# Kernel optimization log

Measured on AMD Instinct MI355X. Metric: run time of the kernel, lower is better.

The kernel has to match this reference:

```python
import jax, jax.numpy as jnp
import numpy as np

N, H, O, E, K = 131072, 128, 128, 8, 2


def setup_inputs() -> dict:
    key = jax.random.key(0)
    k1, k2, k3, k4 = jax.random.split(key, 4)
    x = jax.random.normal(k1, (N, H), dtype=jnp.float32)
    w_gate = jax.random.normal(k2, (H, E), dtype=jnp.float32) * 0.02
    w_noise = jax.random.normal(k3, (H, E), dtype=jnp.float32) * 0.02
    w_expert = jax.random.normal(k4, (E, H, O), dtype=jnp.float32) * (1.0 / np.sqrt(H))
    b_expert = jnp.zeros((E, O), dtype=jnp.float32)
    return {"x": x, "w_gate": w_gate, "w_noise": w_noise,
            "w_expert": w_expert, "b_expert": b_expert, "top_k": K}


def _gates(x, w_gate, top_k):
    # Noisy top-k gating (eval mode: noise term w_noise is inactive).
    logits = x @ w_gate                              # [N, E]
    top_vals, top_idx = jax.lax.top_k(logits, top_k)  # [N, K]
    top_gates = jax.nn.softmax(top_vals, axis=-1)     # renormalize over top-k
    n = logits.shape[0]
    rows = jnp.arange(n)[:, None]                     # [N, 1]
    gates = jnp.zeros_like(logits).at[rows, top_idx].set(top_gates)  # [N, E] sparse
    return gates


def reference(x, w_gate, w_noise, w_expert, b_expert, top_k):
    gates = _gates(x, w_gate, top_k)                                  # [N, E]
    # Dense (mathematically identical) dispatch/combine: every expert FFN
    # applied per token, weighted by its (mostly-zero) gate.
    expert_out = jnp.einsum('nh,eho->neo', x, w_expert) + b_expert     # [N, E, O]
    out = jnp.einsum('ne,neo->no', gates, expert_out)                  # [N, O]
    return out
```

## Files before the change

kernel.cpp:

```cpp
#include <hip/hip_runtime.h>
#include <math.h>

typedef __bf16 bf16x8 __attribute__((ext_vector_type(8)));
typedef float f32x16 __attribute__((ext_vector_type(16)));

#define NTOK 131072
#define HDIM 128
#define ODIM 128
#define NEXP 8

__device__ __forceinline__ unsigned short f2bf(float f){
  union { float f; unsigned u; } v; v.f = f;
  unsigned r = v.u + 0x7FFFu + ((v.u >> 16) & 1u);
  return (unsigned short)(r >> 16);
}

__global__ void pack_w(const float* __restrict__ we, const float* __restrict__ be,
                       unsigned short* __restrict__ pw){
  int f = blockIdx.x * 256 + threadIdx.x;
  int l  = f & 63;
  int kt = (f >> 6) % 9;
  int emt = f / (64 * 9);
  int mt = emt & 3;
  int e  = emt >> 2;
  int o  = (mt << 5) + (l & 31);
  unsigned short vals[8];
#pragma unroll
  for (int j = 0; j < 8; ++j){
    int kl = ((l >> 5) << 3) + j;
    float v;
    if (kt < 8){
      int h = kt * 16 + kl;
      v = we[(e * HDIM + h) * ODIM + o];
    } else {
      v = (kl == 0) ? be[e * ODIM + o] : 0.0f;
    }
    vals[j] = f2bf(v);
  }
  *(bf16x8*)(pw + (size_t)f * 8) = *(bf16x8*)vals;
}

__launch_bounds__(256, 2)
__global__ void moe_fused(const float* __restrict__ x, const float* __restrict__ wg,
                          const unsigned short* __restrict__ pw, float* __restrict__ out){
  __shared__ char lds[33792 + 4096 + 2048];
  float* xs            = (float*)lds;
  unsigned short* frag = (unsigned short*)lds;
  float* tb            = (float*)lds;
  float* wgl           = (float*)(lds + 33792);
  float* glds          = (float*)(lds + 33792 + 4096);

  int t = threadIdx.x;
  size_t tokbase = (size_t)blockIdx.x * 64;

  ((float4*)wgl)[t] = ((const float4*)wg)[t];
  {
    const float4* xsrc = (const float4*)(x + tokbase * HDIM);
#pragma unroll
    for (int i = 0; i < 8; ++i){
      int idx = i * 256 + t;
      int tok = idx >> 5, c = idx & 31;
      *(float4*)&xs[tok * 132 + c * 4] = xsrc[idx];
    }
  }
  __syncthreads();

  float4 cv[8];
#pragma unroll
  for (int i = 0; i < 8; ++i)
    cv[i] = *(float4*)&xs[(t >> 2) * 132 + (t & 3) * 32 + i * 4];

  if (t < 64){
    float lg[8];
#pragma unroll
    for (int e = 0; e < 8; ++e) lg[e] = 0.0f;
#pragma unroll 8
    for (int c = 0; c < 32; ++c){
      float4 v = *(float4*)&xs[t * 132 + c * 4];
      const float* wr = wgl + c * 32;
#pragma unroll
      for (int e = 0; e < 8; ++e)
        lg[e] += v.x * wr[e] + v.y * wr[8 + e] + v.z * wr[16 + e] + v.w * wr[24 + e];
    }
    int i1 = 0; float v1 = lg[0];
#pragma unroll
    for (int e = 1; e < 8; ++e) if (lg[e] > v1){ v1 = lg[e]; i1 = e; }
    int i2 = -1; float v2 = -3.4e38f;
#pragma unroll
    for (int e = 0; e < 8; ++e) if (e != i1 && lg[e] > v2){ v2 = lg[e]; i2 = e; }
    float ex = __expf(v2 - v1);
    float inv = 1.0f / (1.0f + ex);
#pragma unroll
    for (int e = 0; e < 8; ++e)
      glds[e * 64 + t] = (e == i1) ? inv : ((e == i2) ? ex * inv : 0.0f);
  }
  __syncthreads();

  {
    int tokL = t >> 2, q = t & 3, tg = tokL >> 5;
#pragma unroll
    for (int jb = 0; jb < 4; ++jb){
      int h0 = q * 32 + jb * 8;
      int kt = h0 >> 4;
      int lslot = (tokL & 31) + 32 * ((h0 >> 3) & 1);
      float4 a = cv[2 * jb], b = cv[2 * jb + 1];
      unsigned long long lo = (unsigned long long)f2bf(a.x)
                            | ((unsigned long long)f2bf(a.y) << 16)
                            | ((unsigned long long)f2bf(a.z) << 32)
                            | ((unsigned long long)f2bf(a.w) << 48);
      unsigned long long hi = (unsigned long long)f2bf(b.x)
                            | ((unsigned long long)f2bf(b.y) << 16)
                            | ((unsigned long long)f2bf(b.z) << 32)
                            | ((unsigned long long)f2bf(b.w) << 48);
      unsigned long long* dst =
        (unsigned long long*)&frag[(((tg * 9) + kt) * 64 + lslot) * 8];
      dst[0] = lo; dst[1] = hi;
    }
    if (t < 128){
      int btg = t >> 6, bl = t & 63;
      unsigned long long* dst =
        (unsigned long long*)&frag[(((btg * 9) + 8) * 64 + bl) * 8];
      dst[0] = (bl < 32) ? 0x3F80ull : 0ull;
      dst[1] = 0ull;
    }
  }
  __syncthreads();

  int w = t >> 6, l = t & 63, l32 = l & 31, lh = l >> 5;

  bf16x8 xb0[9], xb1[9];
#pragma unroll
  for (int kt = 0; kt < 9; ++kt){
    xb0[kt] = *(const bf16x8*)&frag[((0 * 9 + kt) * 64 + l) * 8];
    xb1[kt] = *(const bf16x8*)&frag[((1 * 9 + kt) * 64 + l) * 8];
  }
  __syncthreads();

  f32x16 zero16;
#pragma unroll
  for (int i = 0; i < 16; ++i) zero16[i] = 0.0f;
  f32x16 tot0 = zero16, tot1 = zero16;

  const bf16x8* pwp = (const bf16x8*)pw;
#pragma unroll 1
  for (int e = 0; e < 8; ++e){
    float g0 = glds[e * 64 + l32];
    float g1 = glds[e * 64 + 32 + l32];
    const bf16x8* ap = pwp + ((size_t)(e * 4 + w) * 9) * 64 + l;
    f32x16 p0 = zero16, p1 = zero16;
#pragma unroll
    for (int kt = 0; kt < 9; ++kt){
      bf16x8 a = ap[kt * 64];
      p0 = __builtin_amdgcn_mfma_f32_32x32x16_bf16(a, xb0[kt], p0, 0, 0, 0);
      p1 = __builtin_amdgcn_mfma_f32_32x32x16_bf16(a, xb1[kt], p1, 0, 0, 0);
    }
#pragma unroll
    for (int r = 0; r < 16; ++r){
      tot0[r] += g0 * p0[r];
      tot1[r] += g1 * p1[r];
    }
  }

  {
#pragma unroll
    for (int rg = 0; rg < 4; ++rg){
      int o = w * 32 + rg * 8 + lh * 4;
      {
        int trow = 0 * 32 + l32;
        int cs = (o >> 2) ^ l32;
        *(float4*)&tb[trow * 128 + cs * 4] =
          make_float4(tot0[rg * 4 + 0], tot0[rg * 4 + 1], tot0[rg * 4 + 2], tot0[rg * 4 + 3]);
      }
      {
        int trow = 1 * 32 + l32;
        int cs = (o >> 2) ^ l32;
        *(float4*)&tb[trow * 128 + cs * 4] =
          make_float4(tot1[rg * 4 + 0], tot1[rg * 4 + 1], tot1[rg * 4 + 2], tot1[rg * 4 + 3]);
      }
    }
  }
  __syncthreads();
#pragma unroll
  for (int i = 0; i < 8; ++i){
    int idx = i * 256 + t;
    int trow = idx >> 5, c = idx & 31;
    int cs = c ^ (trow & 31);
    float4 v = *(float4*)&tb[trow * 128 + cs * 4];
    *(float4*)(out + (tokbase + trow) * ODIM + c * 4) = v;
  }
}

extern "C" void kernel_launch(void* const* d_in, const int* in_sizes, int n_in,
                              void* d_out, int out_size, void* d_ws, size_t ws_size,
                              hipStream_t stream){
  const float* x  = (const float*)d_in[0];
  const float* wg = (const float*)d_in[1];
  const float* we = (const float*)d_in[3];
  const float* be = (const float*)d_in[4];
  float* out = (float*)d_out;

  unsigned short* pw = (unsigned short*)d_ws;

  pack_w   <<<72,   256, 0, stream>>>(we, be, pw);
  moe_fused<<<2048, 256, 0, stream>>>(x, wg, pw, out);
}
```

Baseline: 161.3 us.

## Spread gate logit computation across all threads and prefetch gates into registers

Gate logits were computed by only 64 threads, each doing all 8 experts. Now all 256 threads each compute 2 experts for one token, using a transposed copy of w_gate in LDS, and write the logits to LDS before a single thread-group does top-k and softmax. Gate values are loaded into registers before the expert loop, and the loop is unrolled by 2 so weight loads can overlap across experts. This adds a barrier and the LDS transposed stores, and the unroll raises register pressure under the 2-waves launch bound.

```diff
diff --git a/kernel.cpp b/kernel.cpp
--- a/kernel.cpp
+++ b/kernel.cpp
@@ -47,13 +47,20 @@
   float* xs            = (float*)lds;
   unsigned short* frag = (unsigned short*)lds;
   float* tb            = (float*)lds;
-  float* wgl           = (float*)(lds + 33792);
+  float* wgt           = (float*)(lds + 33792);
   float* glds          = (float*)(lds + 33792 + 4096);
 
   int t = threadIdx.x;
   size_t tokbase = (size_t)blockIdx.x * 64;
 
-  ((float4*)wgl)[t] = ((const float4*)wg)[t];
+  {
+    float4 v = ((const float4*)wg)[t];
+    int h = t >> 1, e0 = (t & 1) * 4;
+    wgt[(e0 + 0) * 128 + h] = v.x;
+    wgt[(e0 + 1) * 128 + h] = v.y;
+    wgt[(e0 + 2) * 128 + h] = v.z;
+    wgt[(e0 + 3) * 128 + h] = v.w;
+  }
   {
     const float4* xsrc = (const float4*)(x + tokbase * HDIM);
 #pragma unroll
@@ -70,18 +77,27 @@
   for (int i = 0; i < 8; ++i)
     cv[i] = *(float4*)&xs[(t >> 2) * 132 + (t & 3) * 32 + i * 4];
 
+  {
+    int tok = t & 63;
+    const float* w0 = wgt + (t >> 6) * 2 * 128;
+    const float* w1 = w0 + 128;
+    float lg0 = 0.0f, lg1 = 0.0f;
+#pragma unroll 8
+    for (int c = 0; c < 32; ++c){
+      float4 v = *(float4*)&xs[tok * 132 + c * 4];
+      lg0 += v.x * w0[c * 4] + v.y * w0[c * 4 + 1] + v.z * w0[c * 4 + 2] + v.w * w0[c * 4 + 3];
+      lg1 += v.x * w1[c * 4] + v.y * w1[c * 4 + 1] + v.z * w1[c * 4 + 2] + v.w * w1[c * 4 + 3];
+    }
+    int e0 = (t >> 6) * 2;
+    glds[e0 * 64 + tok] = lg0;
+    glds[(e0 + 1) * 64 + tok] = lg1;
+  }
+  __syncthreads();
+
   if (t < 64){
     float lg[8];
 #pragma unroll
-    for (int e = 0; e < 8; ++e) lg[e] = 0.0f;
-#pragma unroll 8
-    for (int c = 0; c < 32; ++c){
-      float4 v = *(float4*)&xs[t * 132 + c * 4];
-      const float* wr = wgl + c * 32;
-#pragma unroll
-      for (int e = 0; e < 8; ++e)
-        lg[e] += v.x * wr[e] + v.y * wr[8 + e] + v.z * wr[16 + e] + v.w * wr[24 + e];
-    }
+    for (int e = 0; e < 8; ++e) lg[e] = glds[e * 64 + t];
     int i1 = 0; float v1 = lg[0];
 #pragma unroll
     for (int e = 1; e < 8; ++e) if (lg[e] > v1){ v1 = lg[e]; i1 = e; }
@@ -94,7 +110,6 @@
     for (int e = 0; e < 8; ++e)
       glds[e * 64 + t] = (e == i1) ? inv : ((e == i2) ? ex * inv : 0.0f);
   }
-  __syncthreads();
 
   {
     int tokL = t >> 2, q = t & 3, tg = tokL >> 5;
@@ -136,16 +151,21 @@
   }
   __syncthreads();
 
+  float g0r[8], g1r[8];
+#pragma unroll
+  for (int e = 0; e < 8; ++e){
+    g0r[e] = glds[e * 64 + l32];
+    g1r[e] = glds[e * 64 + 32 + l32];
+  }
+
   f32x16 zero16;
 #pragma unroll
   for (int i = 0; i < 16; ++i) zero16[i] = 0.0f;
   f32x16 tot0 = zero16, tot1 = zero16;
 
   const bf16x8* pwp = (const bf16x8*)pw;
-#pragma unroll 1
+#pragma unroll 2
   for (int e = 0; e < 8; ++e){
-    float g0 = glds[e * 64 + l32];
-    float g1 = glds[e * 64 + 32 + l32];
     const bf16x8* ap = pwp + ((size_t)(e * 4 + w) * 9) * 64 + l;
     f32x16 p0 = zero16, p1 = zero16;
 #pragma unroll
@@ -154,6 +174,7 @@
       p0 = __builtin_amdgcn_mfma_f32_32x32x16_bf16(a, xb0[kt], p0, 0, 0, 0);
       p1 = __builtin_amdgcn_mfma_f32_32x32x16_bf16(a, xb1[kt], p1, 0, 0, 0);
     }
+    float g0 = g0r[e], g1 = g1r[e];
 #pragma unroll
     for (int r = 0; r < 16; ++r){
       tot0[r] += g0 * p0[r];
```

Measured after the change: 161.1 us. No clear change (-0.1%).
